# Performance work log

Measured on AMD Instinct MI355X. Metric: run time of the kernel, lower is better.

The kernel has to match this reference:

```python
import jax, jax.numpy as jnp
import numpy as np

EMBED_DIM = 1024
HEAD_DIM = 64


def setup_inputs() -> dict:
    key = jax.random.key(0)
    ks = jax.random.split(key, 7)
    s_in = EMBED_DIM ** -0.5  # torch Linear default init scale
    x = jax.random.normal(ks[0], (4, 4096, EMBED_DIM), dtype=jnp.float32)
    Wk = jax.random.uniform(ks[1], (HEAD_DIM, EMBED_DIM), jnp.float32, -s_in, s_in)
    bk = jax.random.uniform(ks[2], (HEAD_DIM,), jnp.float32, -s_in, s_in)
    Wq = jax.random.uniform(ks[3], (HEAD_DIM, EMBED_DIM), jnp.float32, -s_in, s_in)
    bq = jax.random.uniform(ks[4], (HEAD_DIM,), jnp.float32, -s_in, s_in)
    Wv = jax.random.uniform(ks[5], (HEAD_DIM, EMBED_DIM), jnp.float32, -s_in, s_in)
    bv = jax.random.uniform(ks[6], (HEAD_DIM,), jnp.float32, -s_in, s_in)
    return {"x": x, "Wq": Wq, "bq": bq, "Wk": Wk, "bk": bk, "Wv": Wv, "bv": bv}


def reference(x, Wq, bq, Wk, bk, Wv, bv):
    # torch Linear: y = x @ W.T + b
    q = jnp.einsum('btc,dc->btd', x, Wq) + bq  # [B,T,D]
    k = jnp.einsum('btc,dc->btd', x, Wk) + bk
    v = jnp.einsum('btc,dc->btd', x, Wv) + bv
    scale = HEAD_DIM ** -0.5
    # NOTE: original divides by scale (multiplies by sqrt(head_dim)) -- faithful
    scores = jnp.einsum('btd,bsd->bts', q, k) / scale  # [B,T,T]
    attn_weights = jax.nn.softmax(scores, axis=-1)
    return jnp.einsum('bts,bsd->btd', attn_weights, v)
```

## Files before the change

### kernel.cpp

```cpp
#include <hip/hip_runtime.h>

#define BATCH 4
#define SEQ   4096
#define CDIM  1024
#define DDIM  64
#define NROW  (BATCH * SEQ)
#define NSPL  8
#define SEG   (NROW * DDIM)

typedef _Float16 f16;
typedef _Float16 f16x8 __attribute__((ext_vector_type(8)));
typedef _Float16 f16x4 __attribute__((ext_vector_type(4)));
typedef __fp16   h16x2 __attribute__((ext_vector_type(2)));
typedef float    f32x4 __attribute__((ext_vector_type(4)));

#define MFMA32(a, b, c) __builtin_amdgcn_mfma_f32_16x16x32_f16((a), (b), (c), 0, 0, 0)
#define MFMA16(a, b, c) __builtin_amdgcn_mfma_f32_16x16x16f16((a), (b), (c), 0, 0, 0)

#define GLDS(g, l)                                                            \
  __builtin_amdgcn_global_load_lds((const __attribute__((address_space(1))) void*)(g), \
                                   (__attribute__((address_space(3))) void*)(l), 16, 0, 0)

#define QSCALE 11.5415603f

__device__ inline f16x8 cvt8(f32x4 a, f32x4 b) {
  h16x2 p0 = __builtin_amdgcn_cvt_pkrtz(a[0], a[1]);
  h16x2 p1 = __builtin_amdgcn_cvt_pkrtz(a[2], a[3]);
  h16x2 p2 = __builtin_amdgcn_cvt_pkrtz(b[0], b[1]);
  h16x2 p3 = __builtin_amdgcn_cvt_pkrtz(b[2], b[3]);
  f16x8 r;
  r[0] = p0[0]; r[1] = p0[1]; r[2] = p1[0]; r[3] = p1[1];
  r[4] = p2[0]; r[5] = p2[1]; r[6] = p3[0]; r[7] = p3[1];
  return r;
}

__device__ inline f16x4 cvt4(float a, float b, float c, float d) {
  h16x2 lo = __builtin_amdgcn_cvt_pkrtz(a, b);
  h16x2 hi = __builtin_amdgcn_cvt_pkrtz(c, d);
  f16x4 r;
  r[0] = lo[0]; r[1] = lo[1]; r[2] = hi[0]; r[3] = hi[1];
  return r;
}

__global__ __launch_bounds__(256) void prep_w_kernel(const float* __restrict__ Wq,
                                                     const float* __restrict__ Wk,
                                                     const float* __restrict__ Wv,
                                                     f16* __restrict__ wf2) {
  const int t = blockIdx.x * 256 + threadIdx.x;
  const int lane = t & 63;
  const int s = t >> 6;
  const int mt = s >> 5, ck = s & 31;
  const int mat = mt >> 2, tile = mt & 3;
  const int n = lane & 15, quad = lane >> 4;
  const float* W = (mat == 0) ? Wq : (mat == 1) ? Wk : Wv;
  const float* src = W + (size_t)(tile * 16 + n) * CDIM + ck * 32 + quad * 8;
  const f32x4 a = *(const f32x4*)src;
  const f32x4 b = *(const f32x4*)(src + 4);
  *(f16x8*)(wf2 + (size_t)t * 8) = cvt8(a, b);
}

__global__ __launch_bounds__(256, 4) void proj_kernel(const float* __restrict__ x,
                                                      const f16* __restrict__ wf2,
                                                      const float* __restrict__ bq,
                                                      const float* __restrict__ bk,
                                                      const float* __restrict__ bv,
                                                      f16* __restrict__ qs,
                                                      f16* __restrict__ ks,
                                                      f16* __restrict__ vc) {
  __shared__ __attribute__((aligned(16))) char lx[3 * 8192];
  const int tid = threadIdx.x, lane = tid & 63, w = tid >> 6;
  const int n = lane & 15, quad = lane >> 4;
  const int rowbase = blockIdx.x * 16;
  const int mtb = 3 * w;

  const float* xsrc[2];
#pragma unroll
  for (int j = 0; j < 2; ++j) {
    const int id = 2 * w + j;
    const int r = id * 2 + (lane >> 5);
    const int c = (lane & 31) ^ r;
    xsrc[j] = x + (size_t)(rowbase + r) * CDIM + c * 4;
  }

  auto issue = [&](int ck, int bufi) {
    char* base = &lx[bufi * 8192];
#pragma unroll
    for (int j = 0; j < 2; ++j)
      GLDS(xsrc[j] + ck * 128, base + (2 * w + j) * 1024);
  };

  const f16* wl = wf2 + (size_t)mtb * 16384 + lane * 8;

  f32x4 acc[3];
#pragma unroll
  for (int i = 0; i < 3; ++i) acc[i] = (f32x4){0.f, 0.f, 0.f, 0.f};

  issue(0, 0);
  issue(1, 1);
  for (int ck = 0; ck < 8; ++ck) {
    const int bufi = ck % 3;
    if (ck + 2 < 8) issue(ck + 2, (ck + 2) % 3);
    if (ck + 2 < 8)      asm volatile("s_waitcnt vmcnt(4)" ::: "memory");
    else if (ck + 1 < 8) asm volatile("s_waitcnt vmcnt(2)" ::: "memory");
    else                 asm volatile("s_waitcnt vmcnt(0)" ::: "memory");
    __builtin_amdgcn_s_barrier();
    __builtin_amdgcn_sched_barrier(0);
    const char* xb = &lx[bufi * 8192] + n * 512;
#pragma unroll
    for (int kk = 0; kk < 4; ++kk) {
      const int c1 = kk * 8 + quad * 2;
      const f32x4 xa = *(const f32x4*)(xb + ((c1 ^ n) << 4));
      const f32x4 xc = *(const f32x4*)(xb + (((c1 + 1) ^ n) << 4));
      const f16x8 af = cvt8(xa, xc);
      const f16* wq = wl + (size_t)(ck * 4 + kk) * 512;
      const f16x8 w0 = *(const f16x8*)(wq);
      const f16x8 w1 = *(const f16x8*)(wq + 16384);
      const f16x8 w2 = *(const f16x8*)(wq + 32768);
      acc[0] = MFMA32(af, w0, acc[0]);
      acc[1] = MFMA32(af, w1, acc[1]);
      acc[2] = MFMA32(af, w2, acc[2]);
    }
    __builtin_amdgcn_s_barrier();
  }

  const int r0 = rowbase + quad * 4;
#pragma unroll
  for (int i2 = 0; i2 < 3; ++i2) {
    const int mt = mtb + i2;
    const int mat = mt >> 2, tile = mt & 3;
    const int d = tile * 16 + n;
    const f32x4 aa = acc[i2];
    if (mat == 0) {
      const float bi = bq[d];
#pragma unroll
      for (int r = 0; r < 4; ++r)
        qs[(size_t)(r0 + r) * DDIM + d] = (f16)((aa[r] + bi) * QSCALE);
    } else if (mat == 1) {
      const float bi = bk[d];
#pragma unroll
      for (int r = 0; r < 4; ++r) {
        const int tt = r0 + r;
        const int col = ((((d >> 3) ^ (tt & 7)) << 3) | (d & 7));
        ks[(size_t)tt * DDIM + col] = (f16)(aa[r] + bi);
      }
    } else {
      const float bi = bv[d];
      const int bb = r0 >> 12;
      const int tl = r0 & (SEQ - 1);
      const int ck2 = tl >> 6;
      const int bsw = (((tl & 63) >> 2) ^ n) << 2;
      *(f16x4*)(vc + ((size_t)(bb * 64 + ck2) * 64 + d) * 64 + bsw) =
          cvt4(aa[0] + bi, aa[1] + bi, aa[2] + bi, aa[3] + bi);
    }
  }
}

template <int NSPLIT>
__global__ __launch_bounds__(256, 3) void attn_kernel(const f16* __restrict__ qs,
                                                      const f16* __restrict__ ks,
                                                      const f16* __restrict__ vc,
                                                      float* __restrict__ outp,
                                                      f16* __restrict__ pacc,
                                                      float* __restrict__ pm,
                                                      float* __restrict__ pl) {
  __shared__ __attribute__((aligned(16))) f16 lk[3 * 4096];
  __shared__ __attribute__((aligned(16))) f16 lv[3 * 4096];
  const int tid = threadIdx.x, lane = tid & 63, w = tid >> 6;
  const int n = lane & 15, quad = lane >> 4;
  const int split = blockIdx.x % NSPLIT;
  const int rowblk = blockIdx.x / NSPLIT;
  const int row0 = rowblk * 128 + w * 32;
  const int bb = row0 >> 12;
  const int kbase = split * (SEQ / NSPLIT);
  const int kc0 = kbase >> 6;
  const int NC = SEQ / NSPLIT / 64;

  const f16* ksb = ks + (size_t)bb * SEQ * DDIM;
  const f16* vcb = vc + (size_t)bb * 64 * 4096;

  auto issue = [&](int c, int bufi) {
#pragma unroll
    for (int i = 0; i < 2; ++i) {
      const int id = 2 * w + i;
      GLDS(ksb + (size_t)(kbase + c * 64) * 64 + id * 512 + lane * 8,
           &lk[bufi * 4096 + id * 512]);
      GLDS(vcb + (size_t)(kc0 + c) * 4096 + id * 512 + lane * 8,
           &lv[bufi * 4096 + id * 512]);
    }
  };

  f16x8 qf[2][2];
#pragma unroll
  for (int g = 0; g < 2; ++g)
#pragma unroll
    for (int hh = 0; hh < 2; ++hh)
      qf[g][hh] = *(const f16x8*)(qs + (size_t)(row0 + g * 16 + n) * DDIM + hh * 32 + quad * 8);

  const int kswz = (quad ^ (n & 7)) << 3;
  int vswz[4];
#pragma unroll
  for (int st = 0; st < 4; ++st) vswz[st] = ((((st << 2) | quad) ^ n) << 2);

  f32x4 acc[2][4];
  float m[2] = {-1e30f, -1e30f}, ll[2] = {0.f, 0.f};
#pragma unroll
  for (int g = 0; g < 2; ++g)
#pragma unroll
    for (int t = 0; t < 4; ++t) acc[g][t] = (f32x4){0.f, 0.f, 0.f, 0.f};

  issue(0, 0);
  issue(1, 1);
  for (int c = 0; c < NC; ++c) {
    const int bufi = c % 3;
    if (c + 2 < NC) issue(c + 2, (c + 2) % 3);
    if (c + 2 < NC)      asm volatile("s_waitcnt vmcnt(8)" ::: "memory");
    else if (c + 1 < NC) asm volatile("s_waitcnt vmcnt(4)" ::: "memory");
    else                 asm volatile("s_waitcnt vmcnt(0)" ::: "memory");
    __builtin_amdgcn_s_barrier();
    __builtin_amdgcn_sched_barrier(0);

    f32x4 s[2][4];
#pragma unroll
    for (int st = 0; st < 4; ++st) {
      const f16* lkr = &lk[bufi * 4096 + (st * 16 + n) * 64];
      const f16x8 klo = *(const f16x8*)(lkr + kswz);
      const f16x8 khi = *(const f16x8*)(lkr + (kswz ^ 32));
#pragma unroll
      for (int g = 0; g < 2; ++g) {
        f32x4 z = (f32x4){0.f, 0.f, 0.f, 0.f};
        z = MFMA32(klo, qf[g][0], z);
        s[g][st] = MFMA32(khi, qf[g][1], z);
      }
    }

    f16x4 pq[2][4];
#pragma unroll
    for (int g = 0; g < 2; ++g) {
      f32x4 mx;
#pragma unroll
      for (int r = 0; r < 4; ++r)
        mx[r] = fmaxf(fmaxf(s[g][0][r], s[g][1][r]), fmaxf(s[g][2][r], s[g][3][r]));
      float mloc = fmaxf(fmaxf(mx[0], mx[1]), fmaxf(mx[2], mx[3]));
      mloc = fmaxf(mloc, __shfl_xor(mloc, 16));
      mloc = fmaxf(mloc, __shfl_xor(mloc, 32));
      const float mnew = fmaxf(m[g], mloc);
      const float alpha = __builtin_amdgcn_exp2f(m[g] - mnew);
      m[g] = mnew;
      float psum = 0.f;
#pragma unroll
      for (int st = 0; st < 4; ++st) {
        f32x4 p;
#pragma unroll
        for (int r = 0; r < 4; ++r) p[r] = __builtin_amdgcn_exp2f(s[g][st][r] - mnew);
        psum += (p[0] + p[1]) + (p[2] + p[3]);
        pq[g][st] = cvt4(p[0], p[1], p[2], p[3]);
      }
      ll[g] = ll[g] * alpha + psum;
#pragma unroll
      for (int t = 0; t < 4; ++t) acc[g][t] *= alpha;
    }

#pragma unroll
    for (int dt = 0; dt < 4; ++dt) {
      const f16* lvr = &lv[bufi * 4096 + (dt * 16 + n) * 64];
#pragma unroll
      for (int st = 0; st < 4; ++st) {
        const f16x4 va = *(const f16x4*)(lvr + vswz[st]);
        acc[0][dt] = MFMA16(va, pq[0][st], acc[0][dt]);
        acc[1][dt] = MFMA16(va, pq[1][st], acc[1][dt]);
      }
    }
    __builtin_amdgcn_s_barrier();
  }

  float lred[2];
#pragma unroll
  for (int g = 0; g < 2; ++g) {
    float l = ll[g];
    l += __shfl_xor(l, 16);
    l += __shfl_xor(l, 32);
    lred[g] = l;
  }

  if (NSPLIT == 1) {
#pragma unroll
    for (int g = 0; g < 2; ++g) {
      const float inv = 1.0f / lred[g];
      const int q = row0 + g * 16 + n;
#pragma unroll
      for (int t = 0; t < 4; ++t) {
        f32x4 o = acc[g][t];
#pragma unroll
        for (int r = 0; r < 4; ++r) o[r] *= inv;
        *(f32x4*)(outp + (size_t)q * DDIM + t * 16 + quad * 4) = o;
      }
    }
  } else {
#pragma unroll
    for (int g = 0; g < 2; ++g) {
      const int q = row0 + g * 16 + n;
#pragma unroll
      for (int t = 0; t < 4; ++t)
        *(f16x4*)(pacc + ((size_t)split * NROW + q) * DDIM + t * 16 + quad * 4) =
            cvt4(acc[g][t][0], acc[g][t][1], acc[g][t][2], acc[g][t][3]);
      if (quad == 0) {
        pm[split * NROW + q] = m[g];
        pl[split * NROW + q] = lred[g];
      }
    }
  }
}

template <int NSPLIT>
__global__ __launch_bounds__(256) void combine_kernel(const f16* __restrict__ pacc,
                                                      const float* __restrict__ pm,
                                                      const float* __restrict__ pl,
                                                      float* __restrict__ out) {
  const int idx = blockIdx.x * 256 + threadIdx.x;
  const int row = idx >> 4;
  const int c = (idx & 15) * 4;
  float mm = pm[row];
#pragma unroll
  for (int s = 1; s < NSPLIT; ++s) mm = fmaxf(mm, pm[s * NROW + row]);
  float L = 0.f;
  f32x4 o = (f32x4){0.f, 0.f, 0.f, 0.f};
#pragma unroll
  for (int s = 0; s < NSPLIT; ++s) {
    const float e = __builtin_amdgcn_exp2f(pm[s * NROW + row] - mm);
    L += pl[s * NROW + row] * e;
    const f16x4 a = *(const f16x4*)(pacc + ((size_t)s * NROW + row) * DDIM + c);
#pragma unroll
    for (int j = 0; j < 4; ++j) o[j] += (float)a[j] * e;
  }
  const float inv = 1.0f / L;
#pragma unroll
  for (int j = 0; j < 4; ++j) o[j] *= inv;
  *(f32x4*)(out + (size_t)row * DDIM + c) = o;
}

extern "C" void kernel_launch(void* const* d_in, const int* in_sizes, int n_in,
                              void* d_out, int out_size, void* d_ws, size_t ws_size,
                              hipStream_t stream) {
  const float* x  = (const float*)d_in[0];
  const float* Wq = (const float*)d_in[1];
  const float* bq = (const float*)d_in[2];
  const float* Wk = (const float*)d_in[3];
  const float* bk = (const float*)d_in[4];
  const float* Wv = (const float*)d_in[5];
  const float* bv = (const float*)d_in[6];
  float* out = (float*)d_out;

  f16* wf2 = (f16*)d_ws;
  f16* qs = wf2 + 3 * 65536;
  f16* ks = qs + (size_t)SEG;
  f16* vc = ks + (size_t)SEG;
  f16* pacc = vc + (size_t)SEG;
  float* pm = (float*)(pacc + (size_t)NSPL * SEG);
  float* pl = pm + (size_t)NSPL * NROW;
  const size_t need = (size_t)((char*)(pl + (size_t)NSPL * NROW) - (char*)d_ws);

  prep_w_kernel<<<dim3(96), dim3(256), 0, stream>>>(Wq, Wk, Wv, wf2);
  proj_kernel<<<dim3(NROW / 16), dim3(256), 0, stream>>>(x, wf2, bq, bk, bv, qs, ks, vc);

  if (ws_size >= need) {
    attn_kernel<NSPL><<<dim3(128 * NSPL), dim3(256), 0, stream>>>(qs, ks, vc, nullptr, pacc, pm, pl);
    combine_kernel<NSPL><<<dim3(NROW * 16 / 256), dim3(256), 0, stream>>>(pacc, pm, pl, out);
  } else {
    attn_kernel<1><<<dim3(128), dim3(256), 0, stream>>>(qs, ks, vc, out, nullptr, nullptr, nullptr);
  }
}
```

Measured before the change: 155.1 us.

## Software-pipeline QK of next chunk with softmax and add lazy rescaling

Restructures the attention loop so the QK^T MFMAs for chunk c+1 are issued before the softmax and PV work of chunk c, with ping-pong score buffers. K and V loads are split so the wait only needs the next chunk's K tiles, and the trailing per-iteration barrier is dropped. The online-softmax rescale of acc and l is skipped when the row max did not grow in any lane. This should hide MFMA and LDS latency behind exp work, at the cost of more live registers and a wave-divergent branch.

```diff
diff --git a/kernel.cpp b/kernel.cpp
--- a/kernel.cpp
+++ b/kernel.cpp
@@ -184,6 +184,10 @@
       const int id = 2 * w + i;
       GLDS(ksb + (size_t)(kbase + c * 64) * 64 + id * 512 + lane * 8,
            &lk[bufi * 4096 + id * 512]);
+    }
+#pragma unroll
+    for (int i = 0; i < 2; ++i) {
+      const int id = 2 * w + i;
       GLDS(vcb + (size_t)(kc0 + c) * 4096 + id * 512 + lane * 8,
            &lv[bufi * 4096 + id * 512]);
     }
@@ -208,18 +212,7 @@
 #pragma unroll
     for (int t = 0; t < 4; ++t) acc[g][t] = (f32x4){0.f, 0.f, 0.f, 0.f};
 
-  issue(0, 0);
-  issue(1, 1);
-  for (int c = 0; c < NC; ++c) {
-    const int bufi = c % 3;
-    if (c + 2 < NC) issue(c + 2, (c + 2) % 3);
-    if (c + 2 < NC)      asm volatile("s_waitcnt vmcnt(8)" ::: "memory");
-    else if (c + 1 < NC) asm volatile("s_waitcnt vmcnt(4)" ::: "memory");
-    else                 asm volatile("s_waitcnt vmcnt(0)" ::: "memory");
-    __builtin_amdgcn_s_barrier();
-    __builtin_amdgcn_sched_barrier(0);
-
-    f32x4 s[2][4];
+  auto qk = [&](int bufi, f32x4 (&sO)[2][4]) {
 #pragma unroll
     for (int st = 0; st < 4; ++st) {
       const f16* lkr = &lk[bufi * 4096 + (st * 16 + n) * 64];
@@ -229,9 +222,21 @@
       for (int g = 0; g < 2; ++g) {
         f32x4 z = (f32x4){0.f, 0.f, 0.f, 0.f};
         z = MFMA32(klo, qf[g][0], z);
-        s[g][st] = MFMA32(khi, qf[g][1], z);
-      }
-    }
+        sO[g][st] = MFMA32(khi, qf[g][1], z);
+      }
+    }
+  };
+
+  auto step = [&](int c, f32x4 (&scur)[2][4], f32x4 (&snxt)[2][4]) {
+    if (c > 0) {
+      __builtin_amdgcn_sched_barrier(0);
+      if (c + 1 < NC) asm volatile("s_waitcnt vmcnt(2)" ::: "memory");
+      else            asm volatile("s_waitcnt vmcnt(0)" ::: "memory");
+      __builtin_amdgcn_s_barrier();
+      __builtin_amdgcn_sched_barrier(0);
+    }
+    if (c + 2 < NC) issue(c + 2, (c + 2) % 3);
+    if (c + 1 < NC) qk((c + 1) % 3, snxt);
 
     f16x4 pq[2][4];
 #pragma unroll
@@ -239,27 +244,32 @@
       f32x4 mx;
 #pragma unroll
       for (int r = 0; r < 4; ++r)
-        mx[r] = fmaxf(fmaxf(s[g][0][r], s[g][1][r]), fmaxf(s[g][2][r], s[g][3][r]));
+        mx[r] = fmaxf(fmaxf(scur[g][0][r], scur[g][1][r]),
+                      fmaxf(scur[g][2][r], scur[g][3][r]));
       float mloc = fmaxf(fmaxf(mx[0], mx[1]), fmaxf(mx[2], mx[3]));
       mloc = fmaxf(mloc, __shfl_xor(mloc, 16));
       mloc = fmaxf(mloc, __shfl_xor(mloc, 32));
-      const float mnew = fmaxf(m[g], mloc);
-      const float alpha = __builtin_amdgcn_exp2f(m[g] - mnew);
-      m[g] = mnew;
+      if (__any(mloc > m[g])) {
+        const float mnew = fmaxf(m[g], mloc);
+        const float alpha = __builtin_amdgcn_exp2f(m[g] - mnew);
+        m[g] = mnew;
+        ll[g] *= alpha;
+#pragma unroll
+        for (int t = 0; t < 4; ++t) acc[g][t] *= alpha;
+      }
       float psum = 0.f;
 #pragma unroll
       for (int st = 0; st < 4; ++st) {
         f32x4 p;
 #pragma unroll
-        for (int r = 0; r < 4; ++r) p[r] = __builtin_amdgcn_exp2f(s[g][st][r] - mnew);
+        for (int r = 0; r < 4; ++r) p[r] = __builtin_amdgcn_exp2f(scur[g][st][r] - m[g]);
         psum += (p[0] + p[1]) + (p[2] + p[3]);
         pq[g][st] = cvt4(p[0], p[1], p[2], p[3]);
       }
-      ll[g] = ll[g] * alpha + psum;
-#pragma unroll
-      for (int t = 0; t < 4; ++t) acc[g][t] *= alpha;
-    }
-
+      ll[g] += psum;
+    }
+
+    const int bufi = c % 3;
 #pragma unroll
     for (int dt = 0; dt < 4; ++dt) {
       const f16* lvr = &lv[bufi * 4096 + (dt * 16 + n) * 64];
@@ -270,7 +280,18 @@
         acc[1][dt] = MFMA16(va, pq[1][st], acc[1][dt]);
       }
     }
-    __builtin_amdgcn_s_barrier();
+  };
+
+  issue(0, 0);
+  issue(1, 1);
+  asm volatile("s_waitcnt vmcnt(2)" ::: "memory");
+  __builtin_amdgcn_s_barrier();
+  __builtin_amdgcn_sched_barrier(0);
+  f32x4 sA[2][4], sB[2][4];
+  qk(0, sA);
+  for (int c = 0; c < NC; c += 2) {
+    step(c, sA, sB);
+    step(c + 1, sB, sA);
   }
 
   float lred[2];
```

Result: slower. 180.4 us (+16.3%).
